# Optimization experiments

Hardware: AMD Instinct MI355X
Metric: run time of the kernel (lower is better)

## Reference

```python
import jax, jax.numpy as jnp
import numpy as np

C = 256       # in_channels
INTER = C // 2
BS = 4        # block_size
BN_EPS = 1e-5


def _conv1x1(x, w, b):
    # x: [N,C,H,W], w: [O,C], b: [O]
    return jnp.einsum('nchw,oc->nohw', x, w) + b[None, :, None, None]


def _maxpool2(x):
    n, c, h, w = x.shape
    return x.reshape(n, c, h // 2, 2, w // 2, 2).max(axis=(3, 5))


def setup_inputs() -> dict:
    key = jax.random.key(0)
    ks = jax.random.split(key, 13)
    p = lambda k, shape, s=0.05: jax.random.normal(k, shape, jnp.float32) * s
    return {
        'x': jax.random.normal(ks[0], (8, C, 128, 128), jnp.float32),
        'theta_w': p(ks[1], (INTER, C)), 'theta_b': p(ks[2], (INTER,)),
        'phi_w': p(ks[3], (INTER, C)), 'phi_b': p(ks[4], (INTER,)),
        'g_w': p(ks[5], (INTER, C)), 'g_b': p(ks[6], (INTER,)),
        'w_w': p(ks[7], (C, INTER)), 'w_b': p(ks[8], (C,)),
        'bn_gamma': p(ks[9], (C,)), 'bn_beta': p(ks[10], (C,)),
        'bn_mean': p(ks[11], (C,)), 'bn_var': jnp.abs(p(ks[12], (C,))) + 1.0,
    }


def reference(x, theta_w, theta_b, phi_w, phi_b, g_w, g_b, w_w, w_b,
              bn_gamma, bn_beta, bn_mean, bn_var):
    b, c, h, w = x.shape
    th, tw = h // BS, w // BS  # tile size (32,32)
    # split into BS*BS non-overlapping tiles, batch them: [b*BS*BS, c, th, tw]
    xb = x.reshape(b, c, BS, th, BS, tw).transpose(0, 2, 4, 1, 3, 5)
    xb = xb.reshape(b * BS * BS, c, th, tw)
    # SNLB (batched over all tiles at once)
    theta = _conv1x1(xb, theta_w, theta_b).reshape(-1, INTER, th * tw).transpose(0, 2, 1)  # [N,q,i]
    phi = _maxpool2(_conv1x1(xb, phi_w, phi_b)).reshape(-1, INTER, (th // 2) * (tw // 2))   # [N,i,k]
    g = _maxpool2(_conv1x1(xb, g_w, g_b)).reshape(-1, INTER, (th // 2) * (tw // 2))
    g = g.transpose(0, 2, 1)                                                                # [N,k,i]
    f = jax.nn.softmax(jnp.einsum('nqi,nik->nqk', theta, phi), axis=-1)                     # [N,q,k]
    y = jnp.einsum('nqk,nki->nqi', f, g).transpose(0, 2, 1).reshape(-1, INTER, th, tw)
    wy = _conv1x1(y, w_w, w_b)
    inv = jax.lax.rsqrt(bn_var + BN_EPS)
    wy = (wy - bn_mean[None, :, None, None]) * (inv * bn_gamma)[None, :, None, None] \
         + bn_beta[None, :, None, None]
    z = wy + xb  # [N,c,th,tw]
    # torch: cat tiles along channel dim (tile-major), then view(b, c, th*BS, -1)
    bf = z.reshape(b, BS * BS * c, th, tw)
    return bf.reshape(b, c, th * BS, -1)
```

## Files before the change

### kernel.cpp

```cpp
#include <hip/hip_runtime.h>
#include <hip/hip_bf16.h>

typedef __bf16 bf16_t;
typedef __bf16 bf16x8 __attribute__((ext_vector_type(8)));
typedef float f32x4 __attribute__((ext_vector_type(4)));

#define LDA 264
#define LDX 520
#define LDT 136
#define LDF 264
#define LDP 136
#define LDG 264

__device__ __forceinline__ float ldin(const void* p, long i, int isbf) {
  if (isbf) {
    unsigned short u = ((const unsigned short*)p)[i];
    unsigned int w = ((unsigned int)u) << 16;
    float f; __builtin_memcpy(&f, &w, 4); return f;
  }
  return ((const float*)p)[i];
}

__device__ __forceinline__ bf16_t f2b(float f) {
  unsigned int u; __builtin_memcpy(&u, &f, 4);
  u += 0x7FFFu + ((u >> 16) & 1u);
  unsigned short h = (unsigned short)(u >> 16);
  bf16_t r; __builtin_memcpy(&r, &h, 2); return r;
}

__device__ __forceinline__ float b2f(bf16_t b) {
  unsigned short h; __builtin_memcpy(&h, &b, 2);
  unsigned int u = ((unsigned int)h) << 16;
  float f; __builtin_memcpy(&f, &u, 4); return f;
}

__device__ __forceinline__ float bb2f(unsigned short h) {
  unsigned int u = ((unsigned int)h) << 16;
  float f; __builtin_memcpy(&f, &u, 4); return f;
}

__device__ __forceinline__ unsigned short bbits(bf16_t b) {
  unsigned short h; __builtin_memcpy(&h, &b, 2); return h;
}

__device__ __forceinline__ void ld4(const void* p, long i, int isbf, float* v) {
  if (isbf) {
    ushort4 u = *(const ushort4*)((const unsigned short*)p + i);
    v[0] = bb2f(u.x); v[1] = bb2f(u.y); v[2] = bb2f(u.z); v[3] = bb2f(u.w);
  } else {
    float4 f = *(const float4*)((const float*)p + i);
    v[0] = f.x; v[1] = f.y; v[2] = f.z; v[3] = f.w;
  }
}

__device__ __forceinline__ f32x4 mfma(bf16x8 a, bf16x8 b, f32x4 c) {
  return __builtin_amdgcn_mfma_f32_16x16x32_bf16(a, b, c, 0, 0, 0);
}

__global__ void kdetect(const unsigned int* x, int* flag) {
  __shared__ int cnt;
  if (threadIdx.x == 0) cnt = 0;
  __syncthreads();
  int local = 0;
  for (int k = 0; k < 4; ++k) {
    unsigned int u = x[threadIdx.x * 4 + k];
    unsigned int e = (u >> 7) & 0xFFu;
    if (e >= 116u && e <= 133u) local++;
  }
  atomicAdd(&cnt, local);
  __syncthreads();
  if (threadIdx.x == 0) *flag = (cnt > 512) ? 1 : 0;
}

__global__ void k0(const void* thw_f, const void* phw, const void* gw, const void* ww_f,
                   const void* wb, const void* gma, const void* bta, const void* mean,
                   const void* var, bf16_t* thwb, bf16_t* phwb, bf16_t* gwb, bf16_t* wwb,
                   float* scw, float* shw, const int* flag) {
  int isbf = *flag;
  int i = blockIdx.x * 256 + threadIdx.x;
  thwb[i] = f2b(ldin(thw_f, i, isbf));
  phwb[i] = f2b(ldin(phw, i, isbf));
  gwb[i]  = f2b(ldin(gw, i, isbf));
  wwb[i]  = f2b(ldin(ww_f, i, isbf));
  if (i < 256) {
    float s = ldin(gma, i, isbf) * rsqrtf(ldin(var, i, isbf) + 1e-5f);
    scw[i] = s;
    shw[i] = (ldin(wb, i, isbf) - ldin(mean, i, isbf)) * s + ldin(bta, i, isbf);
  }
}

__global__ __launch_bounds__(256) void k1(const void* xin, const bf16_t* phwb,
    const bf16_t* gwb, const void* phb, const void* gbb,
    bf16_t* phiH, bf16_t* phiL, bf16_t* gT, const int* flag) {
  int isbf = *flag;
  int wg = blockIdx.x;
  int tile = wg >> 4, j = wg & 15;
  int bi = tile >> 4, t16 = tile & 15, ty = t16 >> 2, tx = t16 & 3;
  long xb = (long)bi * 256 * 16384 + (long)(ty * 32 + 2 * j) * 128 + tx * 32;

  __shared__ __align__(16) bf16_t sX[64 * LDA];

  int tid = threadIdx.x, lane = tid & 63, wv = tid >> 6;
  int qd = lane >> 4, ln = lane & 15, kq = qd * 8;

  {
    int mq = tid & 15, c0 = tid >> 4;
    int ma = (mq >> 3) * 128 + (mq & 7) * 4;
    #pragma unroll
    for (int it = 0; it < 16; ++it) {
      int c = it * 16 + c0;
      float v[4];
      ld4(xin, xb + (long)c * 16384 + ma, isbf, v);
      #pragma unroll
      for (int r = 0; r < 4; ++r) sX[(mq * 4 + r) * LDA + c] = f2b(v[r]);
    }
  }
  __syncthreads();

  f32x4 accP[4][2], accG[4][2];
  for (int mb = 0; mb < 4; ++mb) {
    const bf16_t* A = sX + (mb * 16 + ln) * LDA;
    bf16x8 af[8];
    #pragma unroll
    for (int c = 0; c < 8; ++c) af[c] = *(const bf16x8*)(A + c * 32 + kq);
    #pragma unroll
    for (int h = 0; h < 2; ++h) {
      int nt = wv + h * 4;
      const bf16_t* Bp = phwb + (nt * 16 + ln) * 256;
      const bf16_t* Bg = gwb + (nt * 16 + ln) * 256;
      f32x4 ap = {0.f,0.f,0.f,0.f}, ag = {0.f,0.f,0.f,0.f};
      #pragma unroll
      for (int c = 0; c < 8; ++c) {
        int ko = c * 32 + kq;
        ap = mfma(af[c], *(const bf16x8*)(Bp + ko), ap);
        ag = mfma(af[c], *(const bf16x8*)(Bg + ko), ag);
      }
      accP[mb][h] = ap; accG[mb][h] = ag;
    }
  }

  for (int mb2 = 0; mb2 < 2; ++mb2)
    #pragma unroll
    for (int h = 0; h < 2; ++h) {
      int o = (wv + h * 4) * 16 + ln;
      float pb = ldin(phb, o, isbf), gb2 = ldin(gbb, o, isbf);
      #pragma unroll
      for (int r = 0; r < 4; r += 2) {
        float v = fmaxf(fmaxf(accP[mb2][h][r], accP[mb2][h][r + 1]),
                        fmaxf(accP[mb2 + 2][h][r], accP[mb2 + 2][h][r + 1]));
        float u = fmaxf(fmaxf(accG[mb2][h][r], accG[mb2][h][r + 1]),
                        fmaxf(accG[mb2 + 2][h][r], accG[mb2 + 2][h][r + 1]));
        int cp = mb2 * 8 + qd * 2 + (r >> 1);
        int kpos = j * 16 + cp;
        float pv = v + pb;
        bf16_t hi = f2b(pv);
        phiH[(long)tile * 32768 + kpos * 128 + o] = hi;
        phiL[(long)tile * 32768 + kpos * 128 + o] = f2b(pv - b2f(hi));
        gT[(long)tile * 32768 + (long)o * 256 + kpos] = f2b(u + gb2);
      }
    }
}

__global__ __launch_bounds__(256, 3) void k2(const void* xin, const bf16_t* thwb,
    const void* thb, const bf16_t* phiH, const bf16_t* phiL, const bf16_t* gT,
    const bf16_t* wwb, const float* sc, const float* sh, void* outv, const int* flag) {
  int isbf = *flag;
  int wg = (blockIdx.x & 7) * 512 + (blockIdx.x >> 3);
  int tile = wg >> 5, qb = wg & 31;
  int bi = tile >> 4, t16 = tile & 15, ty = t16 >> 2, tx = t16 & 3;
  long xbase = (long)bi * 256 * 16384 + (long)(ty * 32 + qb) * 128 + tx * 32;

  __shared__ __align__(16) char smem[51200];
  bf16_t* sX   = (bf16_t*)smem;
  bf16_t* sPh  = (bf16_t*)smem;
  bf16_t* sPl  = (bf16_t*)(smem + 8704);
  bf16_t* sG   = (bf16_t*)smem;
  bf16_t* sW   = (bf16_t*)smem;
  bf16_t* sY   = (bf16_t*)(smem + 17408);
  bf16_t* sTh  = (bf16_t*)(smem + 33280);
  bf16_t* sTl  = (bf16_t*)(smem + 41984);
  bf16_t* sF   = (bf16_t*)(smem + 33280);
  float* sredM = (float*)(smem + 50688);
  float* sredS = (float*)(smem + 50944);

  int tid = threadIdx.x, lane = tid & 63, wv = tid >> 6;
  int qd = lane >> 4, ln = lane & 15, kq = qd * 8;
  int ms = wv >> 1, half = wv & 1;
  int m0 = ms * 16 + qd * 4;

  {
    int wq = tid & 7, c0 = tid >> 3;
    #pragma unroll
    for (int it = 0; it < 8; ++it) {
      int c = it * 32 + c0;
      float v[4];
      ld4(xin, xbase + (long)c * 16384 + wq * 4, isbf, v);
      #pragma unroll
      for (int r = 0; r < 4; ++r) {
        bf16_t hi = f2b(v[r]);
        sX[(wq * 4 + r) * LDX + c] = hi;
        sX[(wq * 4 + r) * LDX + 256 + c] = f2b(v[r] - b2f(hi));
      }
    }
  }
  __syncthreads();

  {
    bf16x8 Axf[8];
    #pragma unroll
    for (int t = 0; t < 4; ++t) {
      int tms = t >> 1, tns = (t & 1) * 4 + wv;
      if ((t & 1) == 0) {
        const bf16_t* A = sX + (tms * 16 + ln) * LDX;
        #pragma unroll
        for (int c = 0; c < 8; ++c) Axf[c] = *(const bf16x8*)(A + c * 32 + kq);
      }
      const bf16_t* B = thwb + (tns * 16 + ln) * 256;
      f32x4 a = {0.f,0.f,0.f,0.f};
      #pragma unroll
      for (int c = 0; c < 8; ++c) a = mfma(Axf[c], *(const bf16x8*)(B + c * 32 + kq), a);
      float bias = ldin(thb, tns * 16 + ln, isbf);
      #pragma unroll
      for (int r = 0; r < 4; ++r) {
        float v = a[r] + bias;
        bf16_t hi = f2b(v);
        int mrow = tms * 16 + qd * 4 + r;
        sTh[mrow * LDT + tns * 16 + ln] = hi;
        sTl[mrow * LDT + tns * 16 + ln] = f2b(v - b2f(hi));
      }
    }
  }

  const bf16_t* PH = phiH + (long)tile * 32768;
  const bf16_t* PL = phiL + (long)tile * 32768;
  const bf16_t* GG = gT + (long)tile * 32768;

  uint4 pf0 = *(const uint4*)(PH + tid * 8);
  uint4 pf1 = *(const uint4*)(PH + 2048 + tid * 8);
  uint4 pf2 = *(const uint4*)(PL + tid * 8);
  uint4 pf3 = *(const uint4*)(PL + 2048 + tid * 8);

  f32x4 xres[8];
  #pragma unroll
  for (int c4 = 0; c4 < 4; ++c4) {
    #pragma unroll
    for (int jj = 0; jj < 2; ++jj) {
      int o = c4 * 64 + (half * 2 + jj) * 16 + ln;
      f32x4 xr;
      #pragma unroll
      for (int r = 0; r < 4; ++r)
        xr[r] = b2f(sX[(m0 + r) * LDX + o]) + b2f(sX[(m0 + r) * LDX + 256 + o]);
      xres[c4 * 2 + jj] = xr;
    }
  }
  __syncthreads();

  bf16x8 Ah[4], Al[4];
  {
    const bf16_t* th = sTh + (ms * 16 + ln) * LDT;
    const bf16_t* tl = sTl + (ms * 16 + ln) * LDT;
    #pragma unroll
    for (int c = 0; c < 4; ++c) {
      Ah[c] = *(const bf16x8*)(th + c * 32 + kq);
      Al[c] = *(const bf16x8*)(tl + c * 32 + kq);
    }
  }

  int srow = tid >> 4, scol = (tid & 15) * 8;
  int grow = tid >> 5, gcol = (tid & 31) * 8;

  f32x4 S[8];
  #pragma unroll
  for (int c = 0; c < 8; ++c) {
    *(uint4*)(sPh + srow * LDP + scol) = pf0;
    *(uint4*)(sPh + (srow + 16) * LDP + scol) = pf1;
    *(uint4*)(sPl + srow * LDP + scol) = pf2;
    *(uint4*)(sPl + (srow + 16) * LDP + scol) = pf3;
    if (c < 7) {
      pf0 = *(const uint4*)(PH + (c + 1) * 4096 + tid * 8);
      pf1 = *(const uint4*)(PH + (c + 1) * 4096 + 2048 + tid * 8);
      pf2 = *(const uint4*)(PL + (c + 1) * 4096 + tid * 8);
      pf3 = *(const uint4*)(PL + (c + 1) * 4096 + 2048 + tid * 8);
    } else {
      pf0 = *(const uint4*)(GG + tid * 8);
      pf1 = *(const uint4*)(GG + 2048 + tid * 8);
      pf2 = *(const uint4*)(GG + 4096 + tid * 8);
      pf3 = *(const uint4*)(GG + 6144 + tid * 8);
    }
    __syncthreads();
    const bf16_t* Bh = sPh + (half * 16 + ln) * LDP;
    const bf16_t* Bl = sPl + (half * 16 + ln) * LDP;
    f32x4 a = {0.f,0.f,0.f,0.f};
    #pragma unroll
    for (int kk = 0; kk < 4; ++kk) {
      int ko = kk * 32 + kq;
      bf16x8 bh = *(const bf16x8*)(Bh + ko);
      bf16x8 bl = *(const bf16x8*)(Bl + ko);
      a = mfma(Ah[kk], bl, a);
      a = mfma(Al[kk], bh, a);
      a = mfma(Ah[kk], bh, a);
    }
    S[c] = a;
    __syncthreads();
  }

  float Mr[4], Sr[4], inv4[4];
  #pragma unroll
  for (int r = 0; r < 4; ++r) {
    float m = S[0][r];
    #pragma unroll
    for (int t = 1; t < 8; ++t) m = fmaxf(m, S[t][r]);
    #pragma unroll
    for (int d = 1; d < 16; d <<= 1) m = fmaxf(m, __shfl_xor(m, d, 64));
    Mr[r] = m;
  }
  if (ln == 0) {
    #pragma unroll
    for (int r = 0; r < 4; ++r) sredM[(m0 + r) * 2 + half] = Mr[r];
  }
  __syncthreads();
  #pragma unroll
  for (int r = 0; r < 4; ++r) Mr[r] = fmaxf(Mr[r], sredM[(m0 + r) * 2 + (half ^ 1)]);
  #pragma unroll
  for (int r = 0; r < 4; ++r) {
    float s = 0.f;
    #pragma unroll
    for (int t = 0; t < 8; ++t) { float e = __expf(S[t][r] - Mr[r]); S[t][r] = e; s += e; }
    #pragma unroll
    for (int d = 1; d < 16; d <<= 1) s += __shfl_xor(s, d, 64);
    Sr[r] = s;
  }
  if (ln == 0) {
    #pragma unroll
    for (int r = 0; r < 4; ++r) sredS[(m0 + r) * 2 + half] = Sr[r];
  }
  __syncthreads();
  #pragma unroll
  for (int r = 0; r < 4; ++r) inv4[r] = 1.f / (Sr[r] + sredS[(m0 + r) * 2 + (half ^ 1)]);

  #pragma unroll
  for (int c = 0; c < 8; ++c) {
    int n = c * 32 + half * 16 + ln;
    #pragma unroll
    for (int r = 0; r < 4; ++r)
      sF[(m0 + r) * LDF + n] = f2b(S[c][r] * inv4[r]);
  }
  __syncthreads();

  bf16x8 Fa[8];
  {
    const bf16_t* fa = sF + (ms * 16 + ln) * LDF;
    #pragma unroll
    for (int c = 0; c < 8; ++c) Fa[c] = *(const bf16x8*)(fa + c * 32 + kq);
  }
  #pragma unroll
  for (int c = 0; c < 4; ++c) {
    *(uint4*)(sG + grow * LDG + gcol) = pf0;
    *(uint4*)(sG + (grow + 8) * LDG + gcol) = pf1;
    *(uint4*)(sG + (grow + 16) * LDG + gcol) = pf2;
    *(uint4*)(sG + (grow + 24) * LDG + gcol) = pf3;
    if (c < 3) {
      pf0 = *(const uint4*)(GG + (c + 1) * 8192 + tid * 8);
      pf1 = *(const uint4*)(GG + (c + 1) * 8192 + 2048 + tid * 8);
      pf2 = *(const uint4*)(GG + (c + 1) * 8192 + 4096 + tid * 8);
      pf3 = *(const uint4*)(GG + (c + 1) * 8192 + 6144 + tid * 8);
    } else {
      pf0 = *(const uint4*)(wwb + tid * 8);
      pf1 = *(const uint4*)(wwb + 2048 + tid * 8);
      pf2 = *(const uint4*)(wwb + 4096 + tid * 8);
      pf3 = *(const uint4*)(wwb + 6144 + tid * 8);
    }
    __syncthreads();
    const bf16_t* Bg = sG + (half * 16 + ln) * LDG;
    f32x4 a = {0.f,0.f,0.f,0.f};
    #pragma unroll
    for (int kk = 0; kk < 8; ++kk)
      a = mfma(Fa[kk], *(const bf16x8*)(Bg + kk * 32 + kq), a);
    #pragma unroll
    for (int r = 0; r < 4; ++r)
      sY[(m0 + r) * LDT + c * 32 + half * 16 + ln] = f2b(a[r]);
    __syncthreads();
  }

  bf16x8 Ya[4];
  {
    const bf16_t* ya = sY + (ms * 16 + ln) * LDT;
    #pragma unroll
    for (int kk = 0; kk < 4; ++kk) Ya[kk] = *(const bf16x8*)(ya + kk * 32 + kq);
  }
  #pragma unroll
  for (int c = 0; c < 4; ++c) {
    *(uint4*)(sW + srow * LDP + scol) = pf0;
    *(uint4*)(sW + (srow + 16) * LDP + scol) = pf1;
    *(uint4*)(sW + (srow + 32) * LDP + scol) = pf2;
    *(uint4*)(sW + (srow + 48) * LDP + scol) = pf3;
    if (c < 3) {
      pf0 = *(const uint4*)(wwb + (c + 1) * 8192 + tid * 8);
      pf1 = *(const uint4*)(wwb + (c + 1) * 8192 + 2048 + tid * 8);
      pf2 = *(const uint4*)(wwb + (c + 1) * 8192 + 4096 + tid * 8);
      pf3 = *(const uint4*)(wwb + (c + 1) * 8192 + 6144 + tid * 8);
    }
    __syncthreads();
    #pragma unroll
    for (int jj = 0; jj < 2; ++jj) {
      int nsL = half * 2 + jj;
      const bf16_t* B = sW + (nsL * 16 + ln) * LDP;
      f32x4 a = {0.f,0.f,0.f,0.f};
      #pragma unroll
      for (int kk = 0; kk < 4; ++kk)
        a = mfma(Ya[kk], *(const bf16x8*)(B + kk * 32 + kq), a);
      int o = c * 64 + nsL * 16 + ln;
      float s = sc[o], hh = sh[o];
      f32x4 xr = xres[c * 2 + jj];
      long oi = (long)tile * 262144 + (long)o * 1024 + qb * 32 + m0;
      if (isbf) {
        unsigned short u[4];
        #pragma unroll
        for (int r = 0; r < 4; ++r) u[r] = bbits(f2b(a[r] * s + hh + xr[r]));
        __builtin_memcpy((unsigned short*)outv + oi, u, 8);
      } else {
        float vv[4];
        #pragma unroll
        for (int r = 0; r < 4; ++r) vv[r] = a[r] * s + hh + xr[r];
        __builtin_memcpy((float*)outv + oi, vv, 16);
      }
    }
    __syncthreads();
  }
}

extern "C" void kernel_launch(void* const* d_in, const int* in_sizes, int n_in,
                              void* d_out, int out_size, void* d_ws, size_t ws_size,
                              hipStream_t stream) {
  (void)in_sizes; (void)n_in; (void)out_size; (void)ws_size;
  const void* x    = d_in[0];
  const void* thwf = d_in[1];
  const void* thb  = d_in[2];
  const void* phw  = d_in[3];
  const void* phb  = d_in[4];
  const void* gwf  = d_in[5];
  const void* gbb  = d_in[6];
  const void* wwf  = d_in[7];
  const void* wb   = d_in[8];
  const void* gma  = d_in[9];
  const void* bta  = d_in[10];
  const void* mn   = d_in[11];
  const void* vr   = d_in[12];

  char* ws = (char*)d_ws;
  bf16_t* thwb = (bf16_t*)(ws);
  bf16_t* phwb = (bf16_t*)(ws + 65536);
  bf16_t* gwb  = (bf16_t*)(ws + 131072);
  bf16_t* wwb  = (bf16_t*)(ws + 196608);
  float*  sc   = (float*)(ws + 262144);
  float*  sh   = (float*)(ws + 263168);
  int*    flag = (int*)(ws + 264192);
  bf16_t* phiH = (bf16_t*)(ws + 264448);
  bf16_t* phiL = (bf16_t*)(ws + 264448 + 8388608);
  bf16_t* gT   = (bf16_t*)(ws + 264448 + 16777216);

  kdetect<<<1, 256, 0, stream>>>((const unsigned int*)x, flag);
  k0<<<128, 256, 0, stream>>>(thwf, phw, gwf, wwf, wb, gma, bta, mn, vr,
                              thwb, phwb, gwb, wwb, sc, sh, flag);
  k1<<<2048, 256, 0, stream>>>(x, phwb, gwb, phb, gbb, phiH, phiL, gT, flag);
  k2<<<4096, 256, 0, stream>>>(x, thwb, thb, phiH, phiL, gT, wwb, sc, sh,
                               d_out, flag);
}
```

Baseline: 438.7 us.

## Stage k2 operands via direct global-to-LDS loads with double buffering and XOR swizzle

Replaces register-prefetched uint4 staging of phi, g and W tiles in k2 with global_load_lds transfers into double-buffered 8KB/16KB slabs. Synchronisation now uses explicit vmcnt waits and raw barriers instead of __syncthreads. Padded LDS strides are replaced by XOR swizzles in both k1 and k2, which shrinks shared memory. The output epilogue is deferred until after the W GEMM loop. The aim is to overlap memory traffic with MFMA work and cut bank conflicts, at the cost of fragile hand-counted waitcnt logic.

Result: slower. 451.3 us (+2.9%).

```diff
diff --git a/kernel.cpp b/kernel.cpp
--- a/kernel.cpp
+++ b/kernel.cpp
@@ -4,13 +4,6 @@
 typedef __bf16 bf16_t;
 typedef __bf16 bf16x8 __attribute__((ext_vector_type(8)));
 typedef float f32x4 __attribute__((ext_vector_type(4)));
-
-#define LDA 264
-#define LDX 520
-#define LDT 136
-#define LDF 264
-#define LDP 136
-#define LDG 264
 
 __device__ __forceinline__ float ldin(const void* p, long i, int isbf) {
   if (isbf) {
@@ -55,6 +48,45 @@
 
 __device__ __forceinline__ f32x4 mfma(bf16x8 a, bf16x8 b, f32x4 c) {
   return __builtin_amdgcn_mfma_f32_16x16x32_bf16(a, b, c, 0, 0, 0);
+}
+
+__device__ __forceinline__ void gll16(const void* g, void* l) {
+  __builtin_amdgcn_global_load_lds(
+      reinterpret_cast<const __attribute__((address_space(1))) unsigned int*>(
+          reinterpret_cast<unsigned long long>(g)),
+      reinterpret_cast<__attribute__((address_space(3))) unsigned int*>(
+          (unsigned int)reinterpret_cast<unsigned long long>(l)),
+      16, 0, 0);
+}
+
+__device__ __forceinline__ void stage8(const bf16_t* gbase, int grs, bf16_t* lds,
+                                       int wv, int lane) {
+  int sub = lane >> 4, cb = lane & 15;
+  #pragma unroll
+  for (int j = 0; j < 2; ++j) {
+    int row = wv * 8 + j * 4 + sub;
+    int scb = cb ^ (row & 7);
+    gll16(gbase + (long)row * grs + scb * 8, lds + (wv * 8 + j * 4) * 128);
+  }
+}
+
+template <int N>
+__device__ __forceinline__ void waitbar() {
+  asm volatile("s_waitcnt vmcnt(%0) lgkmcnt(0)" ::"n"(N) : "memory");
+  __builtin_amdgcn_sched_barrier(0);
+  __builtin_amdgcn_s_barrier();
+  __builtin_amdgcn_sched_barrier(0);
+}
+__device__ __forceinline__ void relbar() {
+  __builtin_amdgcn_sched_barrier(0);
+  __builtin_amdgcn_s_barrier();
+  __builtin_amdgcn_sched_barrier(0);
+}
+__device__ __forceinline__ void lgkbar() {
+  asm volatile("s_waitcnt lgkmcnt(0)" ::: "memory");
+  __builtin_amdgcn_sched_barrier(0);
+  __builtin_amdgcn_s_barrier();
+  __builtin_amdgcn_sched_barrier(0);
 }
 
 __global__ void kdetect(const unsigned int* x, int* flag) {
@@ -98,7 +130,7 @@
   int bi = tile >> 4, t16 = tile & 15, ty = t16 >> 2, tx = t16 & 3;
   long xb = (long)bi * 256 * 16384 + (long)(ty * 32 + 2 * j) * 128 + tx * 32;
 
-  __shared__ __align__(16) bf16_t sX[64 * LDA];
+  __shared__ __align__(16) bf16_t sX[64 * 256];
 
   int tid = threadIdx.x, lane = tid & 63, wv = tid >> 6;
   int qd = lane >> 4, ln = lane & 15, kq = qd * 8;
@@ -112,17 +144,22 @@
       float v[4];
       ld4(xin, xb + (long)c * 16384 + ma, isbf, v);
       #pragma unroll
-      for (int r = 0; r < 4; ++r) sX[(mq * 4 + r) * LDA + c] = f2b(v[r]);
+      for (int r = 0; r < 4; ++r) {
+        int m = mq * 4 + r;
+        int s = (((m >> 2) ^ m) & 7) << 3;
+        sX[m * 256 + (c ^ s)] = f2b(v[r]);
+      }
     }
   }
   __syncthreads();
 
   f32x4 accP[4][2], accG[4][2];
   for (int mb = 0; mb < 4; ++mb) {
-    const bf16_t* A = sX + (mb * 16 + ln) * LDA;
+    int row = mb * 16 + ln;
+    int s = (((row >> 2) ^ row) & 7) << 3;
     bf16x8 af[8];
     #pragma unroll
-    for (int c = 0; c < 8; ++c) af[c] = *(const bf16x8*)(A + c * 32 + kq);
+    for (int c = 0; c < 8; ++c) af[c] = *(const bf16x8*)(sX + row * 256 + ((c * 32 + kq) ^ s));
     #pragma unroll
     for (int h = 0; h < 2; ++h) {
       int nt = wv + h * 4;
@@ -170,18 +207,14 @@
   int bi = tile >> 4, t16 = tile & 15, ty = t16 >> 2, tx = t16 & 3;
   long xbase = (long)bi * 256 * 16384 + (long)(ty * 32 + qb) * 128 + tx * 32;
 
-  __shared__ __align__(16) char smem[51200];
-  bf16_t* sX   = (bf16_t*)smem;
-  bf16_t* sPh  = (bf16_t*)smem;
-  bf16_t* sPl  = (bf16_t*)(smem + 8704);
-  bf16_t* sG   = (bf16_t*)smem;
-  bf16_t* sW   = (bf16_t*)smem;
-  bf16_t* sY   = (bf16_t*)(smem + 17408);
-  bf16_t* sTh  = (bf16_t*)(smem + 33280);
-  bf16_t* sTl  = (bf16_t*)(smem + 41984);
-  bf16_t* sF   = (bf16_t*)(smem + 33280);
-  float* sredM = (float*)(smem + 50688);
-  float* sredS = (float*)(smem + 50944);
+  __shared__ __align__(16) char smem[49152];
+  bf16_t* sX  = (bf16_t*)smem;
+  bf16_t* sTh = (bf16_t*)(smem + 32768);
+  bf16_t* sTl = (bf16_t*)(smem + 40960);
+  bf16_t* sF  = (bf16_t*)(smem + 32768);
+  bf16_t* sY  = (bf16_t*)(smem + 16384);
+  float* sredM = (float*)(smem + 24576);
+  float* sredS = (float*)(smem + 24832);
 
   int tid = threadIdx.x, lane = tid & 63, wv = tid >> 6;
   int qd = lane >> 4, ln = lane & 15, kq = qd * 8;
@@ -197,13 +230,16 @@
       ld4(xin, xbase + (long)c * 16384 + wq * 4, isbf, v);
       #pragma unroll
       for (int r = 0; r < 4; ++r) {
+        int m = wq * 4 + r;
+        int s = (((m >> 2) ^ m) & 7) << 3;
+        int cs = c ^ s;
         bf16_t hi = f2b(v[r]);
-        sX[(wq * 4 + r) * LDX + c] = hi;
-        sX[(wq * 4 + r) * LDX + 256 + c] = f2b(v[r] - b2f(hi));
-      }
-    }
-  }
-  __syncthreads();
+        sX[m * 512 + cs] = hi;
+        sX[m * 512 + 256 + cs] = f2b(v[r] - b2f(hi));
+      }
+    }
+  }
+  lgkbar();
 
   {
     bf16x8 Axf[8];
@@ -211,9 +247,11 @@
     for (int t = 0; t < 4; ++t) {
       int tms = t >> 1, tns = (t & 1) * 4 + wv;
       if ((t & 1) == 0) {
-        const bf16_t* A = sX + (tms * 16 + ln) * LDX;
+        int row = tms * 16 + ln;
+        int s = (((row >> 2) ^ row) & 7) << 3;
         #pragma unroll
-        for (int c = 0; c < 8; ++c) Axf[c] = *(const bf16x8*)(A + c * 32 + kq);
+        for (int c = 0; c < 8; ++c)
+          Axf[c] = *(const bf16x8*)(sX + row * 512 + ((c * 32 + kq) ^ s));
       }
       const bf16_t* B = thwb + (tns * 16 + ln) * 256;
       f32x4 a = {0.f,0.f,0.f,0.f};
@@ -225,83 +263,82 @@
         float v = a[r] + bias;
         bf16_t hi = f2b(v);
         int mrow = tms * 16 + qd * 4 + r;
-        sTh[mrow * LDT + tns * 16 + ln] = hi;
-        sTl[mrow * LDT + tns * 16 + ln] = f2b(v - b2f(hi));
-      }
+        int col = (tns * 16 + ln) ^ ((mrow & 7) << 3);
+        sTh[mrow * 128 + col] = hi;
+        sTl[mrow * 128 + col] = f2b(v - b2f(hi));
+      }
+    }
+  }
+
+  f32x4 xres[8];
+  #pragma unroll
+  for (int u = 0; u < 8; ++u) {
+    int o = (2 * u + half) * 16 + ln;
+    f32x4 xr;
+    #pragma unroll
+    for (int r = 0; r < 4; ++r) {
+      int row = m0 + r;
+      int s = (((row >> 2) ^ row) & 7) << 3;
+      int cs = o ^ s;
+      xr[r] = b2f(sX[row * 512 + cs]) + b2f(sX[row * 512 + 256 + cs]);
+    }
+    xres[u] = xr;
+  }
+  lgkbar();
+
+  bf16x8 Ah[4], Al[4];
+  {
+    int row = ms * 16 + ln, sw = (row & 7) << 3;
+    #pragma unroll
+    for (int c = 0; c < 4; ++c) {
+      Ah[c] = *(const bf16x8*)(sTh + row * 128 + ((c * 32 + kq) ^ sw));
+      Al[c] = *(const bf16x8*)(sTl + row * 128 + ((c * 32 + kq) ^ sw));
     }
   }
 
   const bf16_t* PH = phiH + (long)tile * 32768;
   const bf16_t* PL = phiL + (long)tile * 32768;
   const bf16_t* GG = gT + (long)tile * 32768;
-
-  uint4 pf0 = *(const uint4*)(PH + tid * 8);
-  uint4 pf1 = *(const uint4*)(PH + 2048 + tid * 8);
-  uint4 pf2 = *(const uint4*)(PL + tid * 8);
-  uint4 pf3 = *(const uint4*)(PL + 2048 + tid * 8);
-
-  f32x4 xres[8];
-  #pragma unroll
-  for (int c4 = 0; c4 < 4; ++c4) {
-    #pragma unroll
-    for (int jj = 0; jj < 2; ++jj) {
-      int o = c4 * 64 + (half * 2 + jj) * 16 + ln;
-      f32x4 xr;
-      #pragma unroll
-      for (int r = 0; r < 4; ++r)
-        xr[r] = b2f(sX[(m0 + r) * LDX + o]) + b2f(sX[(m0 + r) * LDX + 256 + o]);
-      xres[c4 * 2 + jj] = xr;
-    }
-  }
-  __syncthreads();
-
-  bf16x8 Ah[4], Al[4];
-  {
-    const bf16_t* th = sTh + (ms * 16 + ln) * LDT;
-    const bf16_t* tl = sTl + (ms * 16 + ln) * LDT;
-    #pragma unroll
-    for (int c = 0; c < 4; ++c) {
-      Ah[c] = *(const bf16x8*)(th + c * 32 + kq);
-      Al[c] = *(const bf16x8*)(tl + c * 32 + kq);
-    }
-  }
-
-  int srow = tid >> 4, scol = (tid & 15) * 8;
-  int grow = tid >> 5, gcol = (tid & 31) * 8;
+  bf16_t* slabA = (bf16_t*)smem;
+  bf16_t* slabB = (bf16_t*)(smem + 16384);
+  bf16_t* s8a = (bf16_t*)smem;
+  bf16_t* s8b = (bf16_t*)(smem + 8192);
+
+  stage8(PH, 128, slabA, wv, lane);
+  stage8(PL, 128, slabA + 4096, wv, lane);
+  stage8(PH + 4096, 128, slabB, wv, lane);
+  stage8(PL + 4096, 128, slabB + 4096, wv, lane);
+
+  int brow = half * 16 + ln;
+  int bsw = (brow & 7) << 3;
 
   f32x4 S[8];
   #pragma unroll
   for (int c = 0; c < 8; ++c) {
-    *(uint4*)(sPh + srow * LDP + scol) = pf0;
-    *(uint4*)(sPh + (srow + 16) * LDP + scol) = pf1;
-    *(uint4*)(sPl + srow * LDP + scol) = pf2;
-    *(uint4*)(sPl + (srow + 16) * LDP + scol) = pf3;
-    if (c < 7) {
-      pf0 = *(const uint4*)(PH + (c + 1) * 4096 + tid * 8);
-      pf1 = *(const uint4*)(PH + (c + 1) * 4096 + 2048 + tid * 8);
-      pf2 = *(const uint4*)(PL + (c + 1) * 4096 + tid * 8);
-      pf3 = *(const uint4*)(PL + (c + 1) * 4096 + 2048 + tid * 8);
-    } else {
-      pf0 = *(const uint4*)(GG + tid * 8);
-      pf1 = *(const uint4*)(GG + 2048 + tid * 8);
-      pf2 = *(const uint4*)(GG + 4096 + tid * 8);
-      pf3 = *(const uint4*)(GG + 6144 + tid * 8);
-    }
-    __syncthreads();
-    const bf16_t* Bh = sPh + (half * 16 + ln) * LDP;
-    const bf16_t* Bl = sPl + (half * 16 + ln) * LDP;
+    if (c < 7) waitbar<4>(); else waitbar<2>();
+    const bf16_t* Bh = ((c & 1) ? slabB : slabA) + brow * 128;
+    const bf16_t* Bl = Bh + 4096;
     f32x4 a = {0.f,0.f,0.f,0.f};
     #pragma unroll
     for (int kk = 0; kk < 4; ++kk) {
-      int ko = kk * 32 + kq;
-      bf16x8 bh = *(const bf16x8*)(Bh + ko);
-      bf16x8 bl = *(const bf16x8*)(Bl + ko);
+      int co = (kk * 32 + kq) ^ bsw;
+      bf16x8 bh = *(const bf16x8*)(Bh + co);
+      bf16x8 bl = *(const bf16x8*)(Bl + co);
       a = mfma(Ah[kk], bl, a);
       a = mfma(Al[kk], bh, a);
       a = mfma(Ah[kk], bh, a);
     }
     S[c] = a;
-    __syncthreads();
+    relbar();
+    if (c < 6) {
+      bf16_t* dst = (c & 1) ? slabB : slabA;
+      stage8(PH + (c + 2) * 4096, 128, dst, wv, lane);
+      stage8(PL + (c + 2) * 4096, 128, dst + 4096, wv, lane);
+    } else if (c == 6) {
+      stage8(GG, 256, s8a, wv, lane);
+    } else {
+      stage8(GG + 128, 256, s8b, wv, lane);
+    }
   }
 
   float Mr[4], Sr[4], inv4[4];
@@ -318,7 +355,7 @@
     #pragma unroll
     for (int r = 0; r < 4; ++r) sredM[(m0 + r) * 2 + half] = Mr[r];
   }
-  __syncthreads();
+  lgkbar();
   #pragma unroll
   for (int r = 0; r < 4; ++r) Mr[r] = fmaxf(Mr[r], sredM[(m0 + r) * 2 + (half ^ 1)]);
   #pragma unroll
@@ -334,7 +371,7 @@
     #pragma unroll
     for (int r = 0; r < 4; ++r) sredS[(m0 + r) * 2 + half] = Sr[r];
   }
-  __syncthreads();
+  lgkbar();
   #pragma unroll
   for (int r = 0; r < 4; ++r) inv4[r] = 1.f / (Sr[r] + sredS[(m0 + r) * 2 + (half ^ 1)]);
 
@@ -342,90 +379,90 @@
   for (int c = 0; c < 8; ++c) {
     int n = c * 32 + half * 16 + ln;
     #pragma unroll
-    for (int r = 0; r < 4; ++r)
-      sF[(m0 + r) * LDF + n] = f2b(S[c][r] * inv4[r]);
-  }
-  __syncthreads();
+    for (int r = 0; r < 4; ++r) {
+      int row = m0 + r;
+      sF[row * 256 + (n ^ ((row & 7) << 3))] = f2b(S[c][r] * inv4[r]);
+    }
+  }
+  lgkbar();
 
   bf16x8 Fa[8];
   {
-    const bf16_t* fa = sF + (ms * 16 + ln) * LDF;
-    #pragma unroll
-    for (int c = 0; c < 8; ++c) Fa[c] = *(const bf16x8*)(fa + c * 32 + kq);
-  }
-  #pragma unroll
-  for (int c = 0; c < 4; ++c) {
-    *(uint4*)(sG + grow * LDG + gcol) = pf0;
-    *(uint4*)(sG + (grow + 8) * LDG + gcol) = pf1;
-    *(uint4*)(sG + (grow + 16) * LDG + gcol) = pf2;
-    *(uint4*)(sG + (grow + 24) * LDG + gcol) = pf3;
-    if (c < 3) {
-      pf0 = *(const uint4*)(GG + (c + 1) * 8192 + tid * 8);
-      pf1 = *(const uint4*)(GG + (c + 1) * 8192 + 2048 + tid * 8);
-      pf2 = *(const uint4*)(GG + (c + 1) * 8192 + 4096 + tid * 8);
-      pf3 = *(const uint4*)(GG + (c + 1) * 8192 + 6144 + tid * 8);
+    int row = ms * 16 + ln, sw = (row & 7) << 3;
+    #pragma unroll
+    for (int c = 0; c < 8; ++c)
+      Fa[c] = *(const bf16x8*)(sF + row * 256 + ((c * 32 + kq) ^ sw));
+  }
+
+  f32x4 ya = {0.f,0.f,0.f,0.f};
+  #pragma unroll
+  for (int u = 0; u < 8; ++u) {
+    int ib = u >> 1, kh = u & 1;
+    waitbar<2>();
+    const bf16_t* Bg = ((u & 1) ? s8b : s8a) + brow * 128;
+    if (kh == 0) ya = (f32x4){0.f,0.f,0.f,0.f};
+    #pragma unroll
+    for (int kk = 0; kk < 4; ++kk)
+      ya = mfma(Fa[kh * 4 + kk], *(const bf16x8*)(Bg + ((kk * 32 + kq) ^ bsw)), ya);
+    if (kh == 1) {
+      #pragma unroll
+      for (int r = 0; r < 4; ++r) {
+        int row = m0 + r;
+        int col = ib * 32 + half * 16 + ln;
+        sY[row * 128 + (col ^ ((row & 7) << 3))] = f2b(ya[r]);
+      }
+    }
+    relbar();
+    if (u < 6) {
+      int u2 = u + 2;
+      stage8(GG + (u2 >> 1) * 8192 + (u2 & 1) * 128, 256,
+             (u2 & 1) ? s8b : s8a, wv, lane);
+    } else if (u == 6) {
+      stage8(wwb, 128, s8a, wv, lane);
     } else {
-      pf0 = *(const uint4*)(wwb + tid * 8);
-      pf1 = *(const uint4*)(wwb + 2048 + tid * 8);
-      pf2 = *(const uint4*)(wwb + 4096 + tid * 8);
-      pf3 = *(const uint4*)(wwb + 6144 + tid * 8);
-    }
-    __syncthreads();
-    const bf16_t* Bg = sG + (half * 16 + ln) * LDG;
+      stage8(wwb + 4096, 128, s8b, wv, lane);
+    }
+  }
+
+  bf16x8 Ya[4];
+  #pragma unroll
+  for (int u = 0; u < 8; ++u) {
+    if (u < 7) waitbar<2>(); else waitbar<0>();
+    if (u == 0) {
+      int row = ms * 16 + ln, sw = (row & 7) << 3;
+      #pragma unroll
+      for (int kk = 0; kk < 4; ++kk)
+        Ya[kk] = *(const bf16x8*)(sY + row * 128 + ((kk * 32 + kq) ^ sw));
+    }
+    const bf16_t* Bw = ((u & 1) ? s8b : s8a) + brow * 128;
     f32x4 a = {0.f,0.f,0.f,0.f};
     #pragma unroll
-    for (int kk = 0; kk < 8; ++kk)
-      a = mfma(Fa[kk], *(const bf16x8*)(Bg + kk * 32 + kq), a);
-    #pragma unroll
-    for (int r = 0; r < 4; ++r)
-      sY[(m0 + r) * LDT + c * 32 + half * 16 + ln] = f2b(a[r]);
-    __syncthreads();
-  }
-
-  bf16x8 Ya[4];
-  {
-    const bf16_t* ya = sY + (ms * 16 + ln) * LDT;
-    #pragma unroll
-    for (int kk = 0; kk < 4; ++kk) Ya[kk] = *(const bf16x8*)(ya + kk * 32 + kq);
-  }
-  #pragma unroll
-  for (int c = 0; c < 4; ++c) {
-    *(uint4*)(sW + srow * LDP + scol) = pf0;
-    *(uint4*)(sW + (srow + 16) * LDP + scol) = pf1;
-    *(uint4*)(sW + (srow + 32) * LDP + scol) = pf2;
-    *(uint4*)(sW + (srow + 48) * LDP + scol) = pf3;
-    if (c < 3) {
-      pf0 = *(const uint4*)(wwb + (c + 1) * 8192 + tid * 8);
-      pf1 = *(const uint4*)(wwb + (c + 1) * 8192 + 2048 + tid * 8);
-      pf2 = *(const uint4*)(wwb + (c + 1) * 8192 + 4096 + tid * 8);
-      pf3 = *(const uint4*)(wwb + (c + 1) * 8192 + 6144 + tid * 8);
-    }
-    __syncthreads();
-    #pragma unroll
-    for (int jj = 0; jj < 2; ++jj) {
-      int nsL = half * 2 + jj;
-      const bf16_t* B = sW + (nsL * 16 + ln) * LDP;
-      f32x4 a = {0.f,0.f,0.f,0.f};
-      #pragma unroll
-      for (int kk = 0; kk < 4; ++kk)
-        a = mfma(Ya[kk], *(const bf16x8*)(B + kk * 32 + kq), a);
-      int o = c * 64 + nsL * 16 + ln;
-      float s = sc[o], hh = sh[o];
-      f32x4 xr = xres[c * 2 + jj];
-      long oi = (long)tile * 262144 + (long)o * 1024 + qb * 32 + m0;
-      if (isbf) {
-        unsigned short u[4];
-        #pragma unroll
-        for (int r = 0; r < 4; ++r) u[r] = bbits(f2b(a[r] * s + hh + xr[r]));
-        __builtin_memcpy((unsigned short*)outv + oi, u, 8);
-      } else {
-        float vv[4];
-        #pragma unroll
-        for (int r = 0; r < 4; ++r) vv[r] = a[r] * s + hh + xr[r];
-        __builtin_memcpy((float*)outv + oi, vv, 16);
-      }
-    }
-    __syncthreads();
+    for (int kk = 0; kk < 4; ++kk)
+      a = mfma(Ya[kk], *(const bf16x8*)(Bw + ((kk * 32 + kq) ^ bsw)), a);
+    int o = u * 32 + half * 16 + ln;
+    float s2 = sc[o], hh = sh[o];
+    #pragma unroll
+    for (int r = 0; r < 4; ++r) xres[u][r] = a[r] * s2 + hh + xres[u][r];
+    relbar();
+    if (u < 6) stage8(wwb + (u + 2) * 4096, 128, (u & 1) ? s8b : s8a, wv, lane);
+  }
+
+  long ob = (long)tile * 262144 + qb * 32 + m0;
+  #pragma unroll
+  for (int u = 0; u < 8; ++u) {
+    int o = u * 32 + half * 16 + ln;
+    long oi = ob + (long)o * 1024;
+    if (isbf) {
+      unsigned short uu[4];
+      #pragma unroll
+      for (int r = 0; r < 4; ++r) uu[r] = bbits(f2b(xres[u][r]));
+      __builtin_memcpy((unsigned short*)outv + oi, uu, 8);
+    } else {
+      float vv[4];
+      #pragma unroll
+      for (int r = 0; r < 4; ++r) vv[r] = xres[u][r];
+      __builtin_memcpy((float*)outv + oi, vv, 16);
+    }
   }
 }
 
```

## Swizzle shared x tiles, hoist weight fragments, stage k1 outputs through LDS

Applied to the files above, without the earlier changes.

Replaces the padded shared-memory layouts for the x tile in k1 and k2 with an XOR-swizzled unpadded layout to avoid bank conflicts. In k1, the phi and g weight fragments are kept in registers once per output half instead of being reloaded from global memory for every row block. The pooled phi and g outputs are staged in LDS so they are written to global memory with coalesced 16-byte stores instead of scattered 2-byte stores. This adds LDS usage and register pressure in k1, and a risk of bank conflicts on the narrow store paths to LDS.

Result: no change. 436.9 us (-0.4%).

```diff
diff --git a/kernel.cpp b/kernel.cpp
--- a/kernel.cpp
+++ b/kernel.cpp
@@ -5,8 +5,6 @@
 typedef __bf16 bf16x8 __attribute__((ext_vector_type(8)));
 typedef float f32x4 __attribute__((ext_vector_type(4)));
 
-#define LDA 264
-#define LDX 520
 #define LDT 136
 #define LDF 264
 #define LDP 136
@@ -98,10 +96,24 @@
   int bi = tile >> 4, t16 = tile & 15, ty = t16 >> 2, tx = t16 & 3;
   long xb = (long)bi * 256 * 16384 + (long)(ty * 32 + 2 * j) * 128 + tx * 32;
 
-  __shared__ __align__(16) bf16_t sX[64 * LDA];
+  __shared__ __align__(16) bf16_t sX[64 * 256];
+  __shared__ __align__(16) bf16_t sPoH[16 * 136];
+  __shared__ __align__(16) bf16_t sPoL[16 * 136];
+  __shared__ __align__(16) bf16_t sGo[128 * 24];
 
   int tid = threadIdx.x, lane = tid & 63, wv = tid >> 6;
   int qd = lane >> 4, ln = lane & 15, kq = qd * 8;
+
+  bf16x8 Bp[8], Bg[8];
+  {
+    const bf16_t* bp = phwb + (wv * 16 + ln) * 256;
+    const bf16_t* bg = gwb + (wv * 16 + ln) * 256;
+    #pragma unroll
+    for (int c = 0; c < 8; ++c) {
+      Bp[c] = *(const bf16x8*)(bp + c * 32 + kq);
+      Bg[c] = *(const bf16x8*)(bg + c * 32 + kq);
+    }
+  }
 
   {
     int mq = tid & 15, c0 = tid >> 4;
@@ -112,53 +124,74 @@
       float v[4];
       ld4(xin, xb + (long)c * 16384 + ma, isbf, v);
       #pragma unroll
-      for (int r = 0; r < 4; ++r) sX[(mq * 4 + r) * LDA + c] = f2b(v[r]);
-    }
-  }
-  __syncthreads();
-
-  f32x4 accP[4][2], accG[4][2];
-  for (int mb = 0; mb < 4; ++mb) {
-    const bf16_t* A = sX + (mb * 16 + ln) * LDA;
-    bf16x8 af[8];
-    #pragma unroll
-    for (int c = 0; c < 8; ++c) af[c] = *(const bf16x8*)(A + c * 32 + kq);
-    #pragma unroll
-    for (int h = 0; h < 2; ++h) {
-      int nt = wv + h * 4;
-      const bf16_t* Bp = phwb + (nt * 16 + ln) * 256;
-      const bf16_t* Bg = gwb + (nt * 16 + ln) * 256;
+      for (int r = 0; r < 4; ++r) {
+        int m = mq * 4 + r;
+        int s = (((m >> 2) ^ m) & 7) << 3;
+        sX[m * 256 + (c ^ s)] = f2b(v[r]);
+      }
+    }
+  }
+  __syncthreads();
+
+  #pragma unroll
+  for (int h = 0; h < 2; ++h) {
+    if (h == 1) {
+      const bf16_t* bp = phwb + ((wv + 4) * 16 + ln) * 256;
+      const bf16_t* bg = gwb + ((wv + 4) * 16 + ln) * 256;
+      #pragma unroll
+      for (int c = 0; c < 8; ++c) {
+        Bp[c] = *(const bf16x8*)(bp + c * 32 + kq);
+        Bg[c] = *(const bf16x8*)(bg + c * 32 + kq);
+      }
+    }
+    f32x4 accP[4], accG[4];
+    #pragma unroll
+    for (int mb = 0; mb < 4; ++mb) {
+      int row = mb * 16 + ln;
+      int s = (((row >> 2) ^ row) & 7) << 3;
+      bf16x8 af[8];
+      #pragma unroll
+      for (int c = 0; c < 8; ++c)
+        af[c] = *(const bf16x8*)(sX + row * 256 + ((c * 32 + kq) ^ s));
       f32x4 ap = {0.f,0.f,0.f,0.f}, ag = {0.f,0.f,0.f,0.f};
       #pragma unroll
       for (int c = 0; c < 8; ++c) {
-        int ko = c * 32 + kq;
-        ap = mfma(af[c], *(const bf16x8*)(Bp + ko), ap);
-        ag = mfma(af[c], *(const bf16x8*)(Bg + ko), ag);
-      }
-      accP[mb][h] = ap; accG[mb][h] = ag;
-    }
-  }
-
-  for (int mb2 = 0; mb2 < 2; ++mb2)
-    #pragma unroll
-    for (int h = 0; h < 2; ++h) {
-      int o = (wv + h * 4) * 16 + ln;
-      float pb = ldin(phb, o, isbf), gb2 = ldin(gbb, o, isbf);
+        ap = mfma(af[c], Bp[c], ap);
+        ag = mfma(af[c], Bg[c], ag);
+      }
+      accP[mb] = ap; accG[mb] = ag;
+    }
+    int o = (wv + h * 4) * 16 + ln;
+    float pb = ldin(phb, o, isbf), gb2 = ldin(gbb, o, isbf);
+    #pragma unroll
+    for (int mb2 = 0; mb2 < 2; ++mb2)
       #pragma unroll
       for (int r = 0; r < 4; r += 2) {
-        float v = fmaxf(fmaxf(accP[mb2][h][r], accP[mb2][h][r + 1]),
-                        fmaxf(accP[mb2 + 2][h][r], accP[mb2 + 2][h][r + 1]));
-        float u = fmaxf(fmaxf(accG[mb2][h][r], accG[mb2][h][r + 1]),
-                        fmaxf(accG[mb2 + 2][h][r], accG[mb2 + 2][h][r + 1]));
+        float v = fmaxf(fmaxf(accP[mb2][r], accP[mb2][r + 1]),
+                        fmaxf(accP[mb2 + 2][r], accP[mb2 + 2][r + 1]));
+        float u = fmaxf(fmaxf(accG[mb2][r], accG[mb2][r + 1]),
+                        fmaxf(accG[mb2 + 2][r], accG[mb2 + 2][r + 1]));
         int cp = mb2 * 8 + qd * 2 + (r >> 1);
-        int kpos = j * 16 + cp;
         float pv = v + pb;
         bf16_t hi = f2b(pv);
-        phiH[(long)tile * 32768 + kpos * 128 + o] = hi;
-        phiL[(long)tile * 32768 + kpos * 128 + o] = f2b(pv - b2f(hi));
-        gT[(long)tile * 32768 + (long)o * 256 + kpos] = f2b(u + gb2);
-      }
-    }
+        sPoH[cp * 136 + o] = hi;
+        sPoL[cp * 136 + o] = f2b(pv - b2f(hi));
+        sGo[o * 24 + cp] = f2b(u + gb2);
+      }
+  }
+  __syncthreads();
+
+  {
+    int kp = tid >> 4, seg = tid & 15;
+    long base = (long)tile * 32768 + (long)(j * 16 + kp) * 128 + seg * 8;
+    *(uint4*)(phiH + base) = *(const uint4*)(sPoH + kp * 136 + seg * 8);
+    *(uint4*)(phiL + base) = *(const uint4*)(sPoL + kp * 136 + seg * 8);
+  }
+  {
+    int o = tid >> 1, sg = tid & 1;
+    *(uint4*)(gT + (long)tile * 32768 + (long)o * 256 + j * 16 + sg * 8) =
+        *(const uint4*)(sGo + o * 24 + sg * 8);
+  }
 }
 
 __global__ __launch_bounds__(256, 3) void k2(const void* xin, const bf16_t* thwb,
@@ -197,9 +230,12 @@
       ld4(xin, xbase + (long)c * 16384 + wq * 4, isbf, v);
       #pragma unroll
       for (int r = 0; r < 4; ++r) {
+        int m = wq * 4 + r;
+        int s = (((m >> 2) ^ m) & 7) << 3;
+        int cs = c ^ s;
         bf16_t hi = f2b(v[r]);
-        sX[(wq * 4 + r) * LDX + c] = hi;
-        sX[(wq * 4 + r) * LDX + 256 + c] = f2b(v[r] - b2f(hi));
+        sX[m * 512 + cs] = hi;
+        sX[m * 512 + 256 + cs] = f2b(v[r] - b2f(hi));
       }
     }
   }
@@ -211,9 +247,11 @@
     for (int t = 0; t < 4; ++t) {
       int tms = t >> 1, tns = (t & 1) * 4 + wv;
       if ((t & 1) == 0) {
-        const bf16_t* A = sX + (tms * 16 + ln) * LDX;
+        int row = tms * 16 + ln;
+        int s = (((row >> 2) ^ row) & 7) << 3;
         #pragma unroll
-        for (int c = 0; c < 8; ++c) Axf[c] = *(const bf16x8*)(A + c * 32 + kq);
+        for (int c = 0; c < 8; ++c)
+          Axf[c] = *(const bf16x8*)(sX + row * 512 + ((c * 32 + kq) ^ s));
       }
       const bf16_t* B = thwb + (tns * 16 + ln) * 256;
       f32x4 a = {0.f,0.f,0.f,0.f};
@@ -248,8 +286,12 @@
       int o = c4 * 64 + (half * 2 + jj) * 16 + ln;
       f32x4 xr;
       #pragma unroll
-      for (int r = 0; r < 4; ++r)
-        xr[r] = b2f(sX[(m0 + r) * LDX + o]) + b2f(sX[(m0 + r) * LDX + 256 + o]);
+      for (int r = 0; r < 4; ++r) {
+        int row = m0 + r;
+        int s = (((row >> 2) ^ row) & 7) << 3;
+        int cs = o ^ s;
+        xr[r] = b2f(sX[row * 512 + cs]) + b2f(sX[row * 512 + 256 + cs]);
+      }
       xres[c4 * 2 + jj] = xr;
     }
   }
@@ -389,16 +431,16 @@
     for (int kk = 0; kk < 4; ++kk) Ya[kk] = *(const bf16x8*)(ya + kk * 32 + kq);
   }
   #pragma unroll
-  for (int c = 0; c < 4; ++c) {
+  for (int cb = 0; cb < 4; ++cb) {
     *(uint4*)(sW + srow * LDP + scol) = pf0;
     *(uint4*)(sW + (srow + 16) * LDP + scol) = pf1;
     *(uint4*)(sW + (srow + 32) * LDP + scol) = pf2;
     *(uint4*)(sW + (srow + 48) * LDP + scol) = pf3;
-    if (c < 3) {
-      pf0 = *(const uint4*)(wwb + (c + 1) * 8192 + tid * 8);
-      pf1 = *(const uint4*)(wwb + (c + 1) * 8192 + 2048 + tid * 8);
-      pf2 = *(const uint4*)(wwb + (c + 1) * 8192 + 4096 + tid * 8);
-      pf3 = *(const uint4*)(wwb + (c + 1) * 8192 + 6144 + tid * 8);
+    if (cb < 3) {
+      pf0 = *(const uint4*)(wwb + (cb + 1) * 8192 + tid * 8);
+      pf1 = *(const uint4*)(wwb + (cb + 1) * 8192 + 2048 + tid * 8);
+      pf2 = *(const uint4*)(wwb + (cb + 1) * 8192 + 4096 + tid * 8);
+      pf3 = *(const uint4*)(wwb + (cb + 1) * 8192 + 6144 + tid * 8);
     }
     __syncthreads();
     #pragma unroll
@@ -409,19 +451,19 @@
       #pragma unroll
       for (int kk = 0; kk < 4; ++kk)
         a = mfma(Ya[kk], *(const bf16x8*)(B + kk * 32 + kq), a);
-      int o = c * 64 + nsL * 16 + ln;
-      float s = sc[o], hh = sh[o];
-      f32x4 xr = xres[c * 2 + jj];
+      int o = cb * 64 + nsL * 16 + ln;
+      float s2 = sc[o], hh = sh[o];
+      f32x4 xr = xres[cb * 2 + jj];
       long oi = (long)tile * 262144 + (long)o * 1024 + qb * 32 + m0;
       if (isbf) {
-        unsigned short u[4];
+        unsigned short uu[4];
         #pragma unroll
-        for (int r = 0; r < 4; ++r) u[r] = bbits(f2b(a[r] * s + hh + xr[r]));
-        __builtin_memcpy((unsigned short*)outv + oi, u, 8);
+        for (int r = 0; r < 4; ++r) uu[r] = bbits(f2b(a[r] * s2 + hh + xr[r]));
+        __builtin_memcpy((unsigned short*)outv + oi, uu, 8);
       } else {
         float vv[4];
         #pragma unroll
-        for (int r = 0; r < 4; ++r) vv[r] = a[r] * s + hh + xr[r];
+        for (int r = 0; r < 4; ++r) vv[r] = a[r] * s2 + hh + xr[r];
         __builtin_memcpy((float*)outv + oi, vv, 16);
       }
     }
```
